# Kernel tuning notes

Hardware: AMD Instinct MI355X
Metric: run time of the kernel (lower is better)

Reference implementation:

```python
import jax, jax.numpy as jnp
import numpy as np

NHEAD = 8
K_NEIGH = 16


def setup_inputs() -> dict:
    key = jax.random.key(0)
    ks = jax.random.split(key, 6)
    B, L, D = 4, 4096, 512
    x = jax.random.normal(ks[0], (B, L, D), dtype=jnp.float32)
    positions = jax.random.uniform(ks[1], (B, L, 3), dtype=jnp.float32)
    in_proj_w = jax.random.normal(ks[2], (3 * D, D), dtype=jnp.float32) * 0.02
    in_proj_b = jax.random.normal(ks[3], (3 * D,), dtype=jnp.float32) * 0.02
    out_proj_w = jax.random.normal(ks[4], (D, D), dtype=jnp.float32) * 0.02
    out_proj_b = jax.random.normal(ks[5], (D,), dtype=jnp.float32) * 0.02
    return {"x": x, "positions": positions, "in_proj_w": in_proj_w,
            "in_proj_b": in_proj_b, "out_proj_w": out_proj_w, "out_proj_b": out_proj_b}


def _sparse_attention(x, positions, in_proj_w, in_proj_b, out_proj_w, out_proj_b):
    B, L, D = x.shape
    H, dh = NHEAD, D // NHEAD
    K = min(K_NEIGH, L)
    scale = 1.0 / jnp.sqrt(jnp.asarray(dh, x.dtype))

    # Pairwise distances [B, L, L]; topk smallest -> neighbor indices [B, L, K].
    diff = positions[:, :, None, :] - positions[:, None, :, :]
    dist = jnp.sqrt(jnp.sum(diff * diff, axis=-1))
    _, nbr = jax.lax.top_k(-dist, K)  # [B, L, K]

    Wq, Wk, Wv = in_proj_w[:D], in_proj_w[D:2 * D], in_proj_w[2 * D:]
    bq, bk, bv = in_proj_b[:D], in_proj_b[D:2 * D], in_proj_b[2 * D:]

    # Query is x[b, i] itself (self is always its own nearest neighbor at dist 0),
    # so the selected attention row equals attention with query x[b, i] over neighbors.
    q = ((x @ Wq.T + bq) * scale).reshape(B, L, H, dh)

    # Gather neighbor features: [B, L, K, D]
    b_idx = jnp.arange(B)[:, None, None]
    local_x = x[b_idx, nbr]
    k = (local_x @ Wk.T + bk).reshape(B, L, K, H, dh)
    v = (local_x @ Wv.T + bv).reshape(B, L, K, H, dh)

    scores = jnp.einsum('blhd,blkhd->blhk', q, k)
    attn = jax.nn.softmax(scores, axis=-1)
    ctx = jnp.einsum('blhk,blkhd->blhd', attn, v).reshape(B, L, D)
    out = ctx @ out_proj_w.T + out_proj_b

    # Faithful fallback: if i not among its neighbors, pass through x[b, i].
    is_in = jnp.any(nbr == jnp.arange(L)[None, :, None], axis=-1)  # [B, L]
    return jnp.where(is_in[..., None], out, x)


def reference(x, positions, in_proj_w, in_proj_b, out_proj_w, out_proj_b):
    return _sparse_attention(x, positions, in_proj_w, in_proj_b, out_proj_w, out_proj_b)
```

## Files before the change

kernel.cpp:

```cpp
#include <hip/hip_runtime.h>
#include <cfloat>
#include <cmath>

constexpr int B = 4;
constexpr int L = 4096;
constexpr int D = 512;
constexpr int NH = 8;
constexpr int DH = 64;
constexpr int KN = 16;
constexpr int M = B * L;
constexpr int N_IN = 3 * D;

typedef __attribute__((ext_vector_type(8))) short short8;
typedef __attribute__((ext_vector_type(4))) float f32x4;
typedef unsigned short ushort;

__device__ __forceinline__ ushort f2bf(float f) {
  unsigned u = __float_as_uint(f);
  u = u + 0x7fffu + ((u >> 16) & 1u);
  return (ushort)(u >> 16);
}
__device__ __forceinline__ float bf2f(ushort h) {
  return __uint_as_float(((unsigned)h) << 16);
}
__device__ __forceinline__ float dot8(const uint4 qu, const uint4 ku, float a) {
  a = fmaf(bf2f((ushort)qu.x), bf2f((ushort)ku.x), a);
  a = fmaf(bf2f((ushort)(qu.x >> 16)), bf2f((ushort)(ku.x >> 16)), a);
  a = fmaf(bf2f((ushort)qu.y), bf2f((ushort)ku.y), a);
  a = fmaf(bf2f((ushort)(qu.y >> 16)), bf2f((ushort)(ku.y >> 16)), a);
  a = fmaf(bf2f((ushort)qu.z), bf2f((ushort)ku.z), a);
  a = fmaf(bf2f((ushort)(qu.z >> 16)), bf2f((ushort)(ku.z >> 16)), a);
  a = fmaf(bf2f((ushort)qu.w), bf2f((ushort)ku.w), a);
  a = fmaf(bf2f((ushort)(qu.w >> 16)), bf2f((ushort)(ku.w >> 16)), a);
  return a;
}
__device__ __forceinline__ uint2 pack4hi(const float4 v) {
  uint2 o;
  o.x = (unsigned)f2bf(v.x) | ((unsigned)f2bf(v.y) << 16);
  o.y = (unsigned)f2bf(v.z) | ((unsigned)f2bf(v.w) << 16);
  return o;
}
__device__ __forceinline__ void gload16(const void* g, void* l) {
  __builtin_amdgcn_global_load_lds(
      (const __attribute__((address_space(1))) void*)g,
      (__attribute__((address_space(3))) void*)l, 16, 0, 0);
}

__global__ __launch_bounds__(256) void cvt_x_kernel(const float* __restrict__ in,
                                                    ushort* __restrict__ out) {
  const int n8 = M * D / 8;
  for (int i = blockIdx.x * 256 + threadIdx.x; i < n8; i += gridDim.x * 256) {
    const float4 v0 = reinterpret_cast<const float4*>(in)[i * 2];
    const float4 v1 = reinterpret_cast<const float4*>(in)[i * 2 + 1];
    uint4 o;
    const uint2 a = pack4hi(v0), b2 = pack4hi(v1);
    o.x = a.x; o.y = a.y; o.z = b2.x; o.w = b2.y;
    reinterpret_cast<uint4*>(out)[i] = o;
  }
}

__global__ __launch_bounds__(256) void cvt_w_kernel(const float* __restrict__ in_w,
                                                    const float* __restrict__ out_w,
                                                    ushort* __restrict__ iwh,
                                                    ushort* __restrict__ owh,
                                                    ushort* __restrict__ owl) {
  const int ni8 = N_IN * D / 8;
  const int no8 = D * D / 8;
  for (int i = blockIdx.x * 256 + threadIdx.x; i < ni8 + no8; i += gridDim.x * 256) {
    if (i < ni8) {
      const float4 v0 = reinterpret_cast<const float4*>(in_w)[i * 2];
      const float4 v1 = reinterpret_cast<const float4*>(in_w)[i * 2 + 1];
      uint4 o;
      const uint2 a = pack4hi(v0), b2 = pack4hi(v1);
      o.x = a.x; o.y = a.y; o.z = b2.x; o.w = b2.y;
      reinterpret_cast<uint4*>(iwh)[i] = o;
    } else {
      const int j = i - ni8;
      const float4 v0 = reinterpret_cast<const float4*>(out_w)[j * 2];
      const float4 v1 = reinterpret_cast<const float4*>(out_w)[j * 2 + 1];
      uint4 oh, ol;
      const uint2 a = pack4hi(v0), b2 = pack4hi(v1);
      oh.x = a.x; oh.y = a.y; oh.z = b2.x; oh.w = b2.y;
      const float4 r0 = make_float4(v0.x - bf2f(f2bf(v0.x)), v0.y - bf2f(f2bf(v0.y)),
                                    v0.z - bf2f(f2bf(v0.z)), v0.w - bf2f(f2bf(v0.w)));
      const float4 r1 = make_float4(v1.x - bf2f(f2bf(v1.x)), v1.y - bf2f(f2bf(v1.y)),
                                    v1.z - bf2f(f2bf(v1.z)), v1.w - bf2f(f2bf(v1.w)));
      const uint2 c = pack4hi(r0), d2 = pack4hi(r1);
      ol.x = c.x; ol.y = c.y; ol.z = d2.x; ol.w = d2.y;
      reinterpret_cast<uint4*>(owh)[j] = oh;
      reinterpret_cast<uint4*>(owl)[j] = ol;
    }
  }
}

constexpr int TP = 65;

__global__ __launch_bounds__(512) void topk_kernel(const float* __restrict__ pos,
                                                   int* __restrict__ nbr,
                                                   int* __restrict__ isin) {
  __shared__ float sxT[64 * TP], syT[64 * TP], szT[64 * TP];
  __shared__ unsigned long long lst[8 * 64];
  const int wave = threadIdx.x >> 6;
  const int lane = threadIdx.x & 63;
  const int b = blockIdx.x >> 9;
  const int l = (blockIdx.x & 511) * 8 + wave;
  const int row = b * L + l;

  const float* p = pos + (size_t)b * L * 3;
  for (int i = threadIdx.x; i < L; i += 512) {
    const int a = (i & 63) * TP + (i >> 6);
    sxT[a] = p[3 * i + 0];
    syT[a] = p[3 * i + 1];
    szT[a] = p[3 * i + 2];
  }
  __syncthreads();

  const int qa = (l & 63) * TP + (l >> 6);
  const float qx = sxT[qa], qy = syT[qa], qz = szT[qa];

  float mA = FLT_MAX, mB2 = FLT_MAX, mC = FLT_MAX, mD2 = FLT_MAX;
  const int base = lane * TP;
  for (int j = 0; j < 64; j += 4) {
#define D2(t, acc)                                                   \
    {                                                                \
      const int a = base + j + t;                                    \
      const float dx = qx - sxT[a], dy = qy - syT[a], dz = qz - szT[a]; \
      acc = fminf(acc, fmaf(dx, dx, fmaf(dy, dy, dz * dz)));         \
    }
    D2(0, mA) D2(1, mB2) D2(2, mC) D2(3, mD2)
#undef D2
  }
  const unsigned mbits = __float_as_uint(fminf(fminf(mA, mB2), fminf(mC, mD2)));

  unsigned lo = 1, hi = 0x40400001u;
  while (lo < hi) {
    const unsigned mid = (lo + hi) >> 1;
    const int c = __popcll(__ballot(mbits < mid));
    if (c >= 16) hi = mid; else lo = mid + 1;
  }
  const unsigned P = lo + 16;

  int cnt = 0;
  unsigned long long am = __ballot(mbits < P);
  const unsigned long long below = (1ull << lane) - 1ull;
  while (am) {
    const int pl = (int)__builtin_ctzll(am);
    am &= am - 1;
    const int a = pl * TP + lane;
    const float dx = qx - sxT[a], dy = qy - syT[a], dz = qz - szT[a];
    const float d2 = fmaf(dx, dx, fmaf(dy, dy, dz * dz));
    const bool hit = __float_as_uint(d2) < P;
    const unsigned long long msk = __ballot(hit);
    if (hit) {
      const int slot = cnt + __popcll(msk & below);
      if (slot < 64) {
        const unsigned c = (unsigned)(lane * 64 + pl);
        lst[wave * 64 + slot] =
            ((unsigned long long)__float_as_uint(sqrtf(d2)) << 32) | c;
      }
    }
    cnt += __popcll(msk);
  }
  const int n = min(cnt, 64);

  const unsigned long long mine = (lane < n) ? lst[wave * 64 + lane] : ~0ull;
  int r = 0;
  for (int i = 0; i < n; ++i) r += (lst[wave * 64 + i] < mine) ? 1 : 0;

  const int idx = (int)(unsigned)(mine & 0xffffffffu);
  const bool wr = (lane < n) && (r < 16);
  if (wr) nbr[(size_t)row * KN + r] = idx;
  const unsigned long long hit2 = __ballot(wr && idx == l);
  if (lane == 0) isin[row] = hit2 ? 1 : 0;
}

constexpr int BM = 128, BN = 128, BK = 32;

__global__ __launch_bounds__(256) void gemm_in(const ushort* __restrict__ A,
                                               const ushort* __restrict__ W,
                                               const float* __restrict__ bias,
                                               ushort* __restrict__ qb,
                                               ushort* __restrict__ kb,
                                               ushort* __restrict__ vb) {
  __shared__ ushort Ah[BM * BK];
  __shared__ ushort Bh[BN * BK];

  const int tid = threadIdx.x;
  const int m0 = blockIdx.x * BM;
  const int n0 = blockIdx.y * BN;

  const int wv = tid >> 6;
  const int lane = tid & 63;
  const int sr = wv * 16 + (lane >> 2);
  const int sc = (lane & 3) * 8;
  const ushort* Asrc = A + (size_t)(m0 + sr) * D + sc;
  const ushort* Wsrc = W + (size_t)(n0 + sr) * D + sc;
  ushort* AhB0 = Ah + (wv * 16) * BK;
  ushort* AhB1 = Ah + (wv * 16 + 64) * BK;
  ushort* BhB0 = Bh + (wv * 16) * BK;
  ushort* BhB1 = Bh + (wv * 16 + 64) * BK;

  const int wr0 = (wv >> 1) * 64;
  const int wc0 = (wv & 1) * 64;
  const int fr_row = lane & 15;
  const int kof = (lane >> 4) * 8;

  f32x4 acc[4][4];
#pragma unroll
  for (int i = 0; i < 4; ++i)
#pragma unroll
    for (int j = 0; j < 4; ++j) acc[i][j] = {0.f, 0.f, 0.f, 0.f};

  for (int k0 = 0; k0 < D; k0 += BK) {
    __syncthreads();
    gload16(Asrc + k0, AhB0);
    gload16(Asrc + (size_t)64 * D + k0, AhB1);
    gload16(Wsrc + k0, BhB0);
    gload16(Wsrc + (size_t)64 * D + k0, BhB1);
    __syncthreads();

    short8 ah[4];
#pragma unroll
    for (int fr = 0; fr < 4; ++fr)
      ah[fr] = *reinterpret_cast<const short8*>(&Ah[(wr0 + fr * 16 + fr_row) * BK + kof]);
#pragma unroll
    for (int fc = 0; fc < 4; ++fc) {
      const short8 bh = *reinterpret_cast<const short8*>(&Bh[(wc0 + fc * 16 + fr_row) * BK + kof]);
#pragma unroll
      for (int fr = 0; fr < 4; ++fr)
        acc[fr][fc] = __builtin_amdgcn_mfma_f32_16x16x32_bf16(ah[fr], bh, acc[fr][fc], 0, 0, 0);
    }
  }

  const int region = n0 >> 9;
  ushort* outb = region == 0 ? qb : (region == 1 ? kb : vb);
  const float scl = region == 0 ? 0.125f : 1.0f;
  const int nloc0 = (n0 & 511) + wc0;
#pragma unroll
  for (int fr = 0; fr < 4; ++fr) {
#pragma unroll
    for (int r = 0; r < 4; ++r) {
      const int grow = m0 + wr0 + fr * 16 + (lane >> 4) * 4 + r;
#pragma unroll
      for (int fc = 0; fc < 4; ++fc) {
        const int cc = fc * 16 + (lane & 15);
        const float v = (acc[fr][fc][r] + bias[n0 + wc0 + cc]) * scl;
        outb[(size_t)grow * D + nloc0 + cc] = f2bf(v);
      }
    }
  }
}

__global__ __launch_bounds__(256) void gemm_out(const ushort* __restrict__ A,
                                                const ushort* __restrict__ Wh,
                                                const ushort* __restrict__ Wl,
                                                const float* __restrict__ bias,
                                                float* __restrict__ C,
                                                const float* __restrict__ X,
                                                const int* __restrict__ isin) {
  __shared__ ushort Ah[BM * BK];
  __shared__ ushort Bh[BN * BK];
  __shared__ ushort Bl[BN * BK];

  const int tid = threadIdx.x;
  const int m0 = blockIdx.x * BM;
  const int n0 = blockIdx.y * BN;

  const int wv = tid >> 6;
  const int lane = tid & 63;
  const int sr = wv * 16 + (lane >> 2);
  const int sc = (lane & 3) * 8;
  const ushort* Asrc = A + (size_t)(m0 + sr) * D + sc;
  const ushort* Hsrc = Wh + (size_t)(n0 + sr) * D + sc;
  const ushort* Lsrc = Wl + (size_t)(n0 + sr) * D + sc;
  ushort* AhB0 = Ah + (wv * 16) * BK;
  ushort* AhB1 = Ah + (wv * 16 + 64) * BK;
  ushort* BhB0 = Bh + (wv * 16) * BK;
  ushort* BhB1 = Bh + (wv * 16 + 64) * BK;
  ushort* BlB0 = Bl + (wv * 16) * BK;
  ushort* BlB1 = Bl + (wv * 16 + 64) * BK;

  const int wr0 = (wv >> 1) * 64;
  const int wc0 = (wv & 1) * 64;
  const int fr_row = lane & 15;
  const int kof = (lane >> 4) * 8;

  f32x4 acc[4][4];
#pragma unroll
  for (int i = 0; i < 4; ++i)
#pragma unroll
    for (int j = 0; j < 4; ++j) acc[i][j] = {0.f, 0.f, 0.f, 0.f};

  for (int k0 = 0; k0 < D; k0 += BK) {
    __syncthreads();
    gload16(Asrc + k0, AhB0);
    gload16(Asrc + (size_t)64 * D + k0, AhB1);
    gload16(Hsrc + k0, BhB0);
    gload16(Hsrc + (size_t)64 * D + k0, BhB1);
    gload16(Lsrc + k0, BlB0);
    gload16(Lsrc + (size_t)64 * D + k0, BlB1);
    __syncthreads();

    short8 ah[4];
#pragma unroll
    for (int fr = 0; fr < 4; ++fr)
      ah[fr] = *reinterpret_cast<const short8*>(&Ah[(wr0 + fr * 16 + fr_row) * BK + kof]);
#pragma unroll
    for (int fc = 0; fc < 4; ++fc) {
      const short8 bh = *reinterpret_cast<const short8*>(&Bh[(wc0 + fc * 16 + fr_row) * BK + kof]);
      const short8 bl = *reinterpret_cast<const short8*>(&Bl[(wc0 + fc * 16 + fr_row) * BK + kof]);
#pragma unroll
      for (int fr = 0; fr < 4; ++fr) {
        acc[fr][fc] = __builtin_amdgcn_mfma_f32_16x16x32_bf16(ah[fr], bh, acc[fr][fc], 0, 0, 0);
        acc[fr][fc] = __builtin_amdgcn_mfma_f32_16x16x32_bf16(ah[fr], bl, acc[fr][fc], 0, 0, 0);
      }
    }
  }

#pragma unroll
  for (int fr = 0; fr < 4; ++fr) {
#pragma unroll
    for (int r = 0; r < 4; ++r) {
      const int grow = m0 + wr0 + fr * 16 + (lane >> 4) * 4 + r;
      const int ok = isin[grow];
#pragma unroll
      for (int fc = 0; fc < 4; ++fc) {
        const int gcol = n0 + wc0 + fc * 16 + (lane & 15);
        float v = acc[fr][fc][r] + bias[gcol];
        if (!ok) v = X[(size_t)grow * D + gcol];
        C[(size_t)grow * D + gcol] = v;
      }
    }
  }
}

__global__ __launch_bounds__(256) void attn_kernel(const ushort* __restrict__ qb,
                                                   const ushort* __restrict__ kb,
                                                   const ushort* __restrict__ vb,
                                                   const int* __restrict__ nbr,
                                                   ushort* __restrict__ ctx) {
  __shared__ float sc[4][NH][KN];
  const int wave = threadIdx.x >> 6;
  const int lane = threadIdx.x & 63;
  const int xcd = blockIdx.x & 7;
  const int slot = blockIdx.x >> 3;
  const int b = xcd >> 1;
  const int idx = ((xcd & 1) << 9) + slot;
  const int bl = b * L + idx * 4 + wave;
  const int bbase = b * L;
  const int* nb = nbr + (size_t)bl * KN;

  const int h = lane >> 3;
  const int n0 = lane & 7;

  const ushort* qp = qb + (size_t)bl * D + h * DH;
  uint4 qv[8];
#pragma unroll
  for (int i = 0; i < 8; ++i)
    qv[i] = *reinterpret_cast<const uint4*>(qp + i * 8);

#pragma unroll
  for (int t = 0; t < 2; ++t) {
    const int j = nb[n0 + t * 8];
    const ushort* kr = kb + (size_t)(bbase + j) * D + h * DH;
    float a = 0.f;
#pragma unroll
    for (int i = 0; i < 8; ++i)
      a = dot8(qv[i], *reinterpret_cast<const uint4*>(kr + i * 8), a);
    sc[wave][h][n0 + t * 8] = a;
  }
  __syncthreads();

  float e[KN];
  float mx = -FLT_MAX;
#pragma unroll
  for (int n = 0; n < KN; ++n) mx = fmaxf(mx, sc[wave][h][n]);
  float sum = 0.f;
#pragma unroll
  for (int n = 0; n < KN; ++n) { e[n] = expf(sc[wave][h][n] - mx); sum += e[n]; }
  const float inv = 1.0f / sum;

  const int d0 = (lane & 7) * 8;
  float acc[8];
#pragma unroll
  for (int i = 0; i < 8; ++i) acc[i] = 0.f;
#pragma unroll
  for (int n = 0; n < KN; ++n) {
    const int j = nb[n];
    const uint4 vv = *reinterpret_cast<const uint4*>(
        vb + (size_t)(bbase + j) * D + h * DH + d0);
    const float w = e[n] * inv;
    acc[0] = fmaf(w, bf2f((ushort)vv.x), acc[0]);
    acc[1] = fmaf(w, bf2f((ushort)(vv.x >> 16)), acc[1]);
    acc[2] = fmaf(w, bf2f((ushort)vv.y), acc[2]);
    acc[3] = fmaf(w, bf2f((ushort)(vv.y >> 16)), acc[3]);
    acc[4] = fmaf(w, bf2f((ushort)vv.z), acc[4]);
    acc[5] = fmaf(w, bf2f((ushort)(vv.z >> 16)), acc[5]);
    acc[6] = fmaf(w, bf2f((ushort)vv.w), acc[6]);
    acc[7] = fmaf(w, bf2f((ushort)(vv.w >> 16)), acc[7]);
  }
  uint4 o;
  o.x = (unsigned)f2bf(acc[0]) | ((unsigned)f2bf(acc[1]) << 16);
  o.y = (unsigned)f2bf(acc[2]) | ((unsigned)f2bf(acc[3]) << 16);
  o.z = (unsigned)f2bf(acc[4]) | ((unsigned)f2bf(acc[5]) << 16);
  o.w = (unsigned)f2bf(acc[6]) | ((unsigned)f2bf(acc[7]) << 16);
  *reinterpret_cast<uint4*>(ctx + (size_t)bl * D + h * DH + d0) = o;
}

extern "C" void kernel_launch(void* const* d_in, const int* in_sizes, int n_in,
                              void* d_out, int out_size, void* d_ws, size_t ws_size,
                              hipStream_t stream) {
  const float* x     = (const float*)d_in[0];
  const float* pos   = (const float*)d_in[1];
  const float* in_w  = (const float*)d_in[2];
  const float* in_b  = (const float*)d_in[3];
  const float* out_w = (const float*)d_in[4];
  const float* out_b = (const float*)d_in[5];
  float* out = (float*)d_out;

  const size_t nbr_bytes  = (size_t)M * KN * sizeof(int);
  const size_t isin_bytes = (size_t)M * sizeof(int);
  const size_t half_bytes = (size_t)M * D * sizeof(ushort);
  const size_t iwh_bytes  = (size_t)N_IN * D * sizeof(ushort);
  const size_t ow_bytes   = (size_t)D * D * sizeof(ushort);
  const size_t need = nbr_bytes + isin_bytes + 5 * half_bytes +
                      iwh_bytes + 2 * ow_bytes + 8192;
  if (ws_size < need) return;

  char* w = (char*)d_ws;
  int*    nbr  = (int*)w;    w += (nbr_bytes + 255) & ~(size_t)255;
  int*    isin = (int*)w;    w += (isin_bytes + 255) & ~(size_t)255;
  ushort* xb   = (ushort*)w; w += (half_bytes + 255) & ~(size_t)255;
  ushort* qb   = (ushort*)w; w += (half_bytes + 255) & ~(size_t)255;
  ushort* kb   = (ushort*)w; w += (half_bytes + 255) & ~(size_t)255;
  ushort* vb   = (ushort*)w; w += (half_bytes + 255) & ~(size_t)255;
  ushort* ctxb = (ushort*)w; w += (half_bytes + 255) & ~(size_t)255;
  ushort* iwh  = (ushort*)w; w += (iwh_bytes + 255) & ~(size_t)255;
  ushort* owh  = (ushort*)w; w += (ow_bytes + 255) & ~(size_t)255;
  ushort* owl  = (ushort*)w;

  cvt_x_kernel<<<2048, 256, 0, stream>>>(x, xb);
  cvt_w_kernel<<<512, 256, 0, stream>>>(in_w, out_w, iwh, owh, owl);

  topk_kernel<<<B * (L / 8), 512, 0, stream>>>(pos, nbr, isin);

  gemm_in<<<dim3(M / BM, N_IN / BN), 256, 0, stream>>>(xb, iwh, in_b, qb, kb, vb);

  attn_kernel<<<M / 4, 256, 0, stream>>>(qb, kb, vb, nbr, ctxb);

  gemm_out<<<dim3(M / BM, D / BN), 256, 0, stream>>>(ctxb, owh, owl, out_b, out, x, isin);
}
```

Measured before the change: 179.4 us.

## Reorder attention queries by Morton spatial cell to improve neighbor K/V locality

```diff
diff --git a/kernel.cpp b/kernel.cpp
--- a/kernel.cpp
+++ b/kernel.cpp
@@ -10,6 +10,7 @@
 constexpr int KN = 16;
 constexpr int M = B * L;
 constexpr int N_IN = 3 * D;
+constexpr int NCELL = 512;
 
 typedef __attribute__((ext_vector_type(8))) short short8;
 typedef __attribute__((ext_vector_type(4))) float f32x4;
@@ -44,6 +45,14 @@
   __builtin_amdgcn_global_load_lds(
       (const __attribute__((address_space(1))) void*)g,
       (__attribute__((address_space(3))) void*)l, 16, 0, 0);
+}
+__device__ __forceinline__ int morton3(int x, int y, int z) {
+  int m = 0;
+#pragma unroll
+  for (int i = 0; i < 3; ++i)
+    m |= (((x >> i) & 1) << (3 * i + 2)) | (((y >> i) & 1) << (3 * i + 1)) |
+         (((z >> i) & 1) << (3 * i));
+  return m;
 }
 
 __global__ __launch_bounds__(256) void cvt_x_kernel(const float* __restrict__ in,
@@ -93,6 +102,53 @@
   }
 }
 
+__global__ __launch_bounds__(256) void cell_rank_kernel(const float* __restrict__ pos,
+                                                        int* __restrict__ cellOf,
+                                                        int* __restrict__ rankOf,
+                                                        int* __restrict__ hist) {
+  const int i = blockIdx.x * 256 + threadIdx.x;
+  if (i >= M) return;
+  const float* p = pos + (size_t)i * 3;
+  const int ix = min(7, max(0, (int)(p[0] * 8.f)));
+  const int iy = min(7, max(0, (int)(p[1] * 8.f)));
+  const int iz = min(7, max(0, (int)(p[2] * 8.f)));
+  const int cell = morton3(ix, iy, iz);
+  cellOf[i] = cell;
+  rankOf[i] = atomicAdd(&hist[(i >> 12) * NCELL + cell], 1);
+}
+
+__global__ __launch_bounds__(512) void scan_kernel(const int* __restrict__ hist,
+                                                   int* __restrict__ offs) {
+  __shared__ int tmp[NCELL];
+  const int t = threadIdx.x;
+  for (int b = 0; b < B; ++b) {
+    const int v = hist[b * NCELL + t];
+    int acc = v;
+    tmp[t] = acc;
+    __syncthreads();
+    for (int s = 1; s < NCELL; s <<= 1) {
+      const int o = (t >= s) ? tmp[t - s] : 0;
+      __syncthreads();
+      acc += o;
+      tmp[t] = acc;
+      __syncthreads();
+    }
+    offs[b * NCELL + t] = acc - v;
+    __syncthreads();
+  }
+}
+
+__global__ __launch_bounds__(256) void scatter_kernel(const int* __restrict__ cellOf,
+                                                      const int* __restrict__ rankOf,
+                                                      const int* __restrict__ offs,
+                                                      int* __restrict__ qorder) {
+  const int i = blockIdx.x * 256 + threadIdx.x;
+  if (i >= M) return;
+  const int b = i >> 12;
+  const int slot = offs[b * NCELL + cellOf[i]] + rankOf[i];
+  qorder[b * L + slot] = i & (L - 1);
+}
+
 constexpr int TP = 65;
 
 __global__ __launch_bounds__(512) void topk_kernel(const float* __restrict__ pos,
@@ -338,15 +394,17 @@
                                                    const ushort* __restrict__ kb,
                                                    const ushort* __restrict__ vb,
                                                    const int* __restrict__ nbr,
+                                                   const int* __restrict__ qorder,
                                                    ushort* __restrict__ ctx) {
   __shared__ float sc[4][NH][KN];
   const int wave = threadIdx.x >> 6;
   const int lane = threadIdx.x & 63;
   const int xcd = blockIdx.x & 7;
-  const int slot = blockIdx.x >> 3;
+  const int chunk = blockIdx.x >> 3;
   const int b = xcd >> 1;
-  const int idx = ((xcd & 1) << 9) + slot;
-  const int bl = b * L + idx * 4 + wave;
+  const int slot = ((xcd & 1) * 512 + chunk) * 4 + wave;
+  const int l = qorder[b * L + slot];
+  const int bl = b * L + l;
   const int bbase = b * L;
   const int* nb = nbr + (size_t)bl * KN;
 
@@ -423,30 +481,43 @@
   const size_t half_bytes = (size_t)M * D * sizeof(ushort);
   const size_t iwh_bytes  = (size_t)N_IN * D * sizeof(ushort);
   const size_t ow_bytes   = (size_t)D * D * sizeof(ushort);
+  const size_t sort_bytes = (size_t)M * sizeof(int);
+  const size_t hist_bytes = (size_t)B * NCELL * sizeof(int);
   const size_t need = nbr_bytes + isin_bytes + 5 * half_bytes +
-                      iwh_bytes + 2 * ow_bytes + 8192;
+                      iwh_bytes + 2 * ow_bytes + 4 * sort_bytes +
+                      2 * hist_bytes + 16384;
   if (ws_size < need) return;
 
   char* w = (char*)d_ws;
-  int*    nbr  = (int*)w;    w += (nbr_bytes + 255) & ~(size_t)255;
-  int*    isin = (int*)w;    w += (isin_bytes + 255) & ~(size_t)255;
-  ushort* xb   = (ushort*)w; w += (half_bytes + 255) & ~(size_t)255;
-  ushort* qb   = (ushort*)w; w += (half_bytes + 255) & ~(size_t)255;
-  ushort* kb   = (ushort*)w; w += (half_bytes + 255) & ~(size_t)255;
-  ushort* vb   = (ushort*)w; w += (half_bytes + 255) & ~(size_t)255;
-  ushort* ctxb = (ushort*)w; w += (half_bytes + 255) & ~(size_t)255;
-  ushort* iwh  = (ushort*)w; w += (iwh_bytes + 255) & ~(size_t)255;
-  ushort* owh  = (ushort*)w; w += (ow_bytes + 255) & ~(size_t)255;
-  ushort* owl  = (ushort*)w;
+  int*    nbr    = (int*)w;    w += (nbr_bytes + 255) & ~(size_t)255;
+  int*    isin   = (int*)w;    w += (isin_bytes + 255) & ~(size_t)255;
+  ushort* xb     = (ushort*)w; w += (half_bytes + 255) & ~(size_t)255;
+  ushort* qb     = (ushort*)w; w += (half_bytes + 255) & ~(size_t)255;
+  ushort* kb     = (ushort*)w; w += (half_bytes + 255) & ~(size_t)255;
+  ushort* vb     = (ushort*)w; w += (half_bytes + 255) & ~(size_t)255;
+  ushort* ctxb   = (ushort*)w; w += (half_bytes + 255) & ~(size_t)255;
+  ushort* iwh    = (ushort*)w; w += (iwh_bytes + 255) & ~(size_t)255;
+  ushort* owh    = (ushort*)w; w += (ow_bytes + 255) & ~(size_t)255;
+  ushort* owl    = (ushort*)w; w += (ow_bytes + 255) & ~(size_t)255;
+  int*    cellOf = (int*)w;    w += (sort_bytes + 255) & ~(size_t)255;
+  int*    rankOf = (int*)w;    w += (sort_bytes + 255) & ~(size_t)255;
+  int*    qorder = (int*)w;    w += (sort_bytes + 255) & ~(size_t)255;
+  int*    hist   = (int*)w;    w += (hist_bytes + 255) & ~(size_t)255;
+  int*    offs   = (int*)w;
 
   cvt_x_kernel<<<2048, 256, 0, stream>>>(x, xb);
   cvt_w_kernel<<<512, 256, 0, stream>>>(in_w, out_w, iwh, owh, owl);
 
+  hipMemsetAsync(hist, 0, hist_bytes, stream);
+  cell_rank_kernel<<<M / 256, 256, 0, stream>>>(pos, cellOf, rankOf, hist);
+  scan_kernel<<<1, NCELL, 0, stream>>>(hist, offs);
+  scatter_kernel<<<M / 256, 256, 0, stream>>>(cellOf, rankOf, offs, qorder);
+
   topk_kernel<<<B * (L / 8), 512, 0, stream>>>(pos, nbr, isin);
 
   gemm_in<<<dim3(M / BM, N_IN / BN), 256, 0, stream>>>(xb, iwh, in_b, qb, kb, vb);
 
-  attn_kernel<<<M / 4, 256, 0, stream>>>(qb, kb, vb, nbr, ctxb);
+  attn_kernel<<<M / 4, 256, 0, stream>>>(qb, kb, vb, nbr, qorder, ctxb);
 
   gemm_out<<<dim3(M / BM, D / BN), 256, 0, stream>>>(ctxb, owh, owl, out_b, out, x, isin);
 }
```

Result: slower. 183.3 us (+2.2%).
